# Optimization experiments

Hardware: AMD Instinct MI355X
Metric: run time of the kernel (lower is better)

Reference implementation:

```python
import jax, jax.numpy as jnp
import numpy as np

NEG_SLOPE = 0.2  # PyG GATConv default negative_slope


def gat_layer(x, src, dst, N, W, att_src, att_dst, bias, heads, out_ch, concat):
    # x: [N, Fin]; W: [Fin, heads*out_ch]; att_*: [heads, out_ch]; bias matches output dim
    h = (x @ W).reshape(N, heads, out_ch)              # [N, H, C]
    a_src = (h * att_src).sum(-1)                      # [N, H]
    a_dst = (h * att_dst).sum(-1)                      # [N, H]
    e = jax.nn.leaky_relu(a_src[src] + a_dst[dst], NEG_SLOPE)  # [E, H]
    # segment softmax over incoming edges of each destination node
    e_max = jax.ops.segment_max(e, dst, num_segments=N)        # [N, H]
    e_exp = jnp.exp(e - e_max[dst])                             # [E, H]
    denom = jax.ops.segment_sum(e_exp, dst, num_segments=N)    # [N, H]
    alpha = e_exp / (denom[dst] + 1e-16)                        # [E, H]
    msg = alpha[:, :, None] * h[src]                            # [E, H, C]
    out = jax.ops.segment_sum(msg, dst, num_segments=N)        # [N, H, C]
    out = out.reshape(N, heads * out_ch) if concat else out.mean(axis=1)
    return out + bias


def setup_inputs() -> dict:
    key = jax.random.key(0)
    ks = jax.random.split(key, 10)
    N, E = 40000, 160000
    Fin, H1, C1 = 602, 8, 256
    H2, C2 = 1, 42
    g = lambda k, shape, fan: (jax.random.normal(k, shape, dtype=jnp.float32) * (1.0 / np.sqrt(fan)))
    return {
        "x": jax.random.normal(ks[0], (N, Fin), dtype=jnp.float32),
        "edge_index": jax.random.randint(ks[1], (2, E), 0, N, dtype=jnp.int64),
        "W1": g(ks[2], (Fin, H1 * C1), Fin),
        "att_src1": g(ks[3], (H1, C1), C1),
        "att_dst1": g(ks[4], (H1, C1), C1),
        "b1": jnp.zeros((H1 * C1,), dtype=jnp.float32),
        "W2": g(ks[5], (H1 * C1, H2 * C2), H1 * C1),
        "att_src2": g(ks[6], (H2, C2), C2),
        "att_dst2": g(ks[7], (H2, C2), C2),
        "b2": jnp.zeros((C2,), dtype=jnp.float32),
    }


def reference(x, edge_index, W1, att_src1, att_dst1, b1, W2, att_src2, att_dst2, b2):
    N = x.shape[0]
    # PyG GATConv default add_self_loops=True
    loops = jnp.arange(N, dtype=edge_index.dtype)
    src = jnp.concatenate([edge_index[0], loops])
    dst = jnp.concatenate([edge_index[1], loops])
    h = gat_layer(x, src, dst, N, W1, att_src1, att_dst1, b1, heads=8, out_ch=256, concat=True)
    h = jax.nn.relu(h)  # dropout is identity in eval mode
    h = gat_layer(h, src, dst, N, W2, att_src2, att_dst2, b2, heads=1, out_ch=42, concat=False)
    return jax.nn.log_softmax(h, axis=1)
```

## Files before the change

kernel.cpp:

```cpp
#include <hip/hip_runtime.h>
#include <hip/hip_bf16.h>

#define NN   40000
#define NE   160000
#define ETOT 200000
#define FIN  602
#define NH1  8
#define C1   256
#define F1   2048
#define C2   42
#define NEG  0.2f
#define NB   157
#define KP   608
#define MP   40192

typedef unsigned short u16;
typedef unsigned int   u32;
typedef __bf16 bf16x8 __attribute__((ext_vector_type(8)));
typedef float  f32x4  __attribute__((ext_vector_type(4)));

__device__ __forceinline__ float bfu(u16 v){ return __uint_as_float(((u32)v) << 16); }
__device__ __forceinline__ float bflo(u32 u){ return __uint_as_float(u << 16); }
__device__ __forceinline__ float bfhi(u32 u){ return __uint_as_float(u & 0xffff0000u); }
__device__ __forceinline__ u16 f2bf(float f){
  u32 u = __float_as_uint(f);
  u32 r = (u + 0x7fffu + ((u >> 16) & 1u)) >> 16;
  return (u16)r;
}

__device__ __forceinline__ void gl_lds16(const u16* g, u16* l) {
  __builtin_amdgcn_global_load_lds(
      (const __attribute__((address_space(1))) u32*)(g),
      (__attribute__((address_space(3))) u32*)(l), 16, 0, 0);
}

__global__ void probe_k(const u32* __restrict__ xw, const int* __restrict__ ei,
                        int* __restrict__ flags) {
  if (threadIdx.x == 0) {
    int zc = 0;
    for (int k = 0; k < 64; ++k) zc += (ei[2*k + 1] == 0) ? 1 : 0;
    flags[0] = (zc == 64) ? 1 : 0;
    int inr = 0;
    for (int k = 0; k < 64; ++k) {
      u32 low = xw[k] & 0xffffu;
      int e = (int)((low >> 7) & 0xff);
      inr += (e >= 100 && e <= 140) ? 1 : 0;
    }
    flags[1] = (inr >= 32) ? 0 : 1;
  }
}

__global__ void cvt_f32_k(const void* __restrict__ src, float* __restrict__ dst, int n,
                          const int* __restrict__ flags) {
  int i = blockIdx.x * 256 + threadIdx.x;
  if (i >= n) return;
  dst[i] = flags[1] ? ((const float*)src)[i] : bfu(((const u16*)src)[i]);
}

__global__ void xb_k(const void* __restrict__ x, u16* __restrict__ xb,
                     const int* __restrict__ flags) {
  int k = blockIdx.x * 256 + threadIdx.x;
  int row = blockIdx.y;
  if (k >= KP) return;
  u16 v = 0;
  if (row < NN && k < FIN)
    v = flags[1] ? f2bf(((const float*)x)[(size_t)row * FIN + k])
                 : ((const u16*)x)[(size_t)row * FIN + k];
  xb[(size_t)row * KP + k] = v;
}

__global__ void w1t_k(const void* __restrict__ W1, u16* __restrict__ w1t,
                      const int* __restrict__ flags) {
  int n = blockIdx.x * 256 + threadIdx.x;
  int k = blockIdx.y;
  if (n >= F1) return;
  u16 v = 0;
  if (k < FIN) v = flags[1] ? f2bf(((const float*)W1)[(size_t)k * F1 + n])
                            : ((const u16*)W1)[(size_t)k * F1 + n];
  w1t[(size_t)n * KP + k] = v;
}

__global__ void w2t_k(const void* __restrict__ W2, u16* __restrict__ w2t,
                      const int* __restrict__ flags) {
  int i = blockIdx.x * 256 + threadIdx.x;
  if (i >= 64 * F1) return;
  int c = i >> 11, k = i & (F1 - 1);
  u16 v = 0;
  if (c < C2) v = flags[1] ? f2bf(((const float*)W2)[(size_t)k * C2 + c])
                           : ((const u16*)W2)[(size_t)k * C2 + c];
  w2t[i] = v;
}

__device__ __forceinline__ void edge_sd(const int* __restrict__ ei, int e, int imode,
                                        int& s, int& d) {
  if (e < NE) {
    if (imode) { s = ei[2*e]; d = ei[2*(NE + e)]; }
    else       { s = ei[e];   d = ei[NE + e];     }
  } else { s = d = e - NE; }
}

__global__ void deg_k(const int* __restrict__ ei, int* __restrict__ deg,
                      const int* __restrict__ flags) {
  int e = blockIdx.x * 256 + threadIdx.x;
  if (e >= ETOT) return;
  int s, d; edge_sd(ei, e, flags[0], s, d);
  atomicAdd(&deg[d], 1);
}

__global__ __launch_bounds__(256) void scan1_k(const int* __restrict__ deg,
                                               int* __restrict__ tmp, int* __restrict__ bsum) {
  __shared__ int s[256];
  int b = blockIdx.x, t = threadIdx.x, i = b * 256 + t;
  int v = (i < NN) ? deg[i] : 0;
  s[t] = v; __syncthreads();
  for (int o = 1; o < 256; o <<= 1) {
    int u = (t >= o) ? s[t - o] : 0;
    __syncthreads(); s[t] += u; __syncthreads();
  }
  if (i < NN) tmp[i] = s[t];
  if (t == 255) bsum[b] = s[255];
}

__global__ __launch_bounds__(256) void scan2_k(int* __restrict__ bsum) {
  __shared__ int s[256];
  int t = threadIdx.x;
  int v = (t < NB) ? bsum[t] : 0;
  s[t] = v; __syncthreads();
  for (int o = 1; o < 256; o <<= 1) {
    int u = (t >= o) ? s[t - o] : 0;
    __syncthreads(); s[t] += u; __syncthreads();
  }
  if (t < NB) bsum[t] = s[t];
}

__global__ void scan3_k(const int* __restrict__ deg, const int* __restrict__ tmp,
                        const int* __restrict__ bsum, int* __restrict__ start, int* __restrict__ cur) {
  int i = blockIdx.x * 256 + threadIdx.x;
  if (i >= NN) return;
  int b = i >> 8;
  int off = b ? bsum[b - 1] : 0;
  int excl = tmp[i] - deg[i] + off;
  start[i] = excl; cur[i] = excl;
}

__global__ void fill_k(const int* __restrict__ ei, int* __restrict__ cur,
                       int* __restrict__ csr_src, int* __restrict__ csr_dst,
                       const int* __restrict__ flags) {
  int e = blockIdx.x * 256 + threadIdx.x;
  if (e >= ETOT) return;
  int s, d; edge_sd(ei, e, flags[0], s, d);
  int pos = atomicAdd(&cur[d], 1);
  csr_src[pos] = s; csr_dst[pos] = d;
}

__global__ __launch_bounds__(512) void gemm1c_k(const u16* __restrict__ xb,
                                                const u16* __restrict__ w1t,
                                                u16* __restrict__ h1,
                                                const float* __restrict__ as1c,
                                                const float* __restrict__ ad1c,
                                                float* __restrict__ a_s1,
                                                float* __restrict__ a_d1) {
  __shared__ u16 As[2 * 8192];
  __shared__ u16 Bs[2 * 8192];
  const int t = threadIdx.x;
  const int lane = t & 63, wid = t >> 6;
  const int wr = wid >> 2, wc = wid & 3;
  const int m0 = blockIdx.y * 256, n0 = blockIdx.x * 256;
  const int l16 = lane & 15;
  f32x4 acc[8][4];
  #pragma unroll
  for (int i = 0; i < 8; ++i)
    #pragma unroll
    for (int j = 0; j < 4; ++j) acc[i][j] = (f32x4){0.f, 0.f, 0.f, 0.f};

  const int kc = ((t & 3) ^ ((t >> 3) & 3)) * 8;
  const size_t sa0 = (size_t)(m0 + (t >> 2)) * KP + kc;
  const size_t sa1 = sa0 + (size_t)128 * KP;
  const size_t sb0 = (size_t)(n0 + (t >> 2)) * KP + kc;
  const size_t sb1 = sb0 + (size_t)128 * KP;

  const int fsw = ((lane >> 4) ^ ((l16 >> 1) & 3)) << 3;
  const int rdA = (wr * 128 + l16) * 32 + fsw;
  const int rdB = (wc * 64 + l16) * 32 + fsw;

#define STAGE(K0, B) do {                                  \
    u16* a_ = As + (B) * 8192 + (wid << 9);                \
    u16* b_ = Bs + (B) * 8192 + (wid << 9);                \
    gl_lds16(xb  + sa0 + (K0), a_);                        \
    gl_lds16(xb  + sa1 + (K0), a_ + 4096);                 \
    gl_lds16(w1t + sb0 + (K0), b_);                        \
    gl_lds16(w1t + sb1 + (K0), b_ + 4096);                 \
  } while (0)

  STAGE(0, 0);
  __syncthreads();
  int cur = 0;
  for (int k0 = 0; k0 < KP; k0 += 32) {
    if (k0 + 32 < KP) STAGE(k0 + 32, cur ^ 1);
    const u16* Ab = As + cur * 8192;
    const u16* Bb = Bs + cur * 8192;
    bf16x8 bfr[4];
    #pragma unroll
    for (int ni = 0; ni < 4; ++ni)
      bfr[ni] = *(const bf16x8*)&Bb[rdB + ni * 512];
    #pragma unroll
    for (int mi = 0; mi < 8; ++mi) {
      bf16x8 af = *(const bf16x8*)&Ab[rdA + mi * 512];
      #pragma unroll
      for (int ni = 0; ni < 4; ++ni)
        acc[mi][ni] = __builtin_amdgcn_mfma_f32_16x16x32_bf16(af, bfr[ni], acc[mi][ni], 0, 0, 0);
    }
    __syncthreads();
    cur ^= 1;
  }
#undef STAGE

  const int h0 = n0 >> 8;
  const int lr4 = (lane >> 4) * 4;
  #pragma unroll
  for (int mi = 0; mi < 8; ++mi) {
    float ps[4] = {0.f, 0.f, 0.f, 0.f}, pd[4] = {0.f, 0.f, 0.f, 0.f};
    #pragma unroll
    for (int ni = 0; ni < 4; ++ni) {
      int col = n0 + wc * 64 + ni * 16 + l16;
      float wsv = as1c[col], wdv = ad1c[col];
      #pragma unroll
      for (int r = 0; r < 4; ++r) {
        float v = acc[mi][ni][r];
        ps[r] += v * wsv;
        pd[r] += v * wdv;
      }
    }
    #pragma unroll
    for (int o = 1; o < 16; o <<= 1) {
      #pragma unroll
      for (int r = 0; r < 4; ++r) {
        ps[r] += __shfl_xor(ps[r], o, 64);
        pd[r] += __shfl_xor(pd[r], o, 64);
      }
    }
    int rowb = m0 + wr * 128 + mi * 16 + lr4;
    if (l16 == 0) {
      #pragma unroll
      for (int r = 0; r < 4; ++r) {
        int row = rowb + r;
        if (row < NN) {
          atomicAdd(&a_s1[row * NH1 + h0], ps[r]);
          atomicAdd(&a_d1[row * NH1 + h0], pd[r]);
        }
      }
    }
    #pragma unroll
    for (int r = 0; r < 4; ++r) {
      int row = rowb + r;
      if (row < NN) {
        #pragma unroll
        for (int ni = 0; ni < 4; ++ni) {
          int col = n0 + wc * 64 + ni * 16 + l16;
          h1[(size_t)row * F1 + col] = f2bf(acc[mi][ni][r]);
        }
      }
    }
  }
}

__global__ __launch_bounds__(256) void gemm1m_k(const void* __restrict__ xv,
                                                const u16* __restrict__ w1t,
                                                u16* __restrict__ h1,
                                                const int* __restrict__ flags) {
  __shared__ u16 As[128][40];
  __shared__ u16 Bs[128][40];
  const int fm = flags[1];
  const int t = threadIdx.x;
  const int lane = t & 63, wid = t >> 6;
  const int wr = wid >> 1, wc = wid & 1;
  const int m0 = blockIdx.y * 128, n0 = blockIdx.x * 128;
  const int l16 = lane & 15, lk = (lane >> 4) * 8;
  f32x4 acc[4][4];
  #pragma unroll
  for (int i = 0; i < 4; ++i)
    #pragma unroll
    for (int j = 0; j < 4; ++j) acc[i][j] = (f32x4){0.f, 0.f, 0.f, 0.f};
  const int arow = t >> 2;
  const int akb  = (t & 3) * 8;
  for (int k0 = 0; k0 < KP; k0 += 32) {
    #pragma unroll
    for (int i = 0; i < 2; ++i) {
      int row = arow + i * 64;
      int rg = m0 + row;
      u32 d0 = 0, d1 = 0, d2 = 0, d3 = 0;
      if (rg < NN) {
        if (k0 + 32 <= FIN) {
          if (fm) {
            const float* xp = (const float*)xv + (size_t)rg * FIN + k0 + akb;
            float2 p0 = *(const float2*)(xp);
            float2 p1 = *(const float2*)(xp + 2);
            float2 p2 = *(const float2*)(xp + 4);
            float2 p3 = *(const float2*)(xp + 6);
            d0 = (u32)f2bf(p0.x) | ((u32)f2bf(p0.y) << 16);
            d1 = (u32)f2bf(p1.x) | ((u32)f2bf(p1.y) << 16);
            d2 = (u32)f2bf(p2.x) | ((u32)f2bf(p2.y) << 16);
            d3 = (u32)f2bf(p3.x) | ((u32)f2bf(p3.y) << 16);
          } else {
            const u16* xp = (const u16*)xv + (size_t)rg * FIN + k0 + akb;
            d0 = *(const u32*)(xp);
            d1 = *(const u32*)(xp + 2);
            d2 = *(const u32*)(xp + 4);
            d3 = *(const u32*)(xp + 6);
          }
        } else {
          u16 e[8];
          #pragma unroll
          for (int q = 0; q < 8; ++q) {
            int k = k0 + akb + q;
            e[q] = 0;
            if (k < FIN)
              e[q] = fm ? f2bf(((const float*)xv)[(size_t)rg * FIN + k])
                        : ((const u16*)xv)[(size_t)rg * FIN + k];
          }
          d0 = (u32)e[0] | ((u32)e[1] << 16);
          d1 = (u32)e[2] | ((u32)e[3] << 16);
          d2 = (u32)e[4] | ((u32)e[5] << 16);
          d3 = (u32)e[6] | ((u32)e[7] << 16);
        }
      }
      *(uint4*)&As[row][akb] = make_uint4(d0, d1, d2, d3);
      const u16* wp = w1t + (size_t)(n0 + row) * KP + k0 + akb;
      *(uint4*)&Bs[row][akb] = *(const uint4*)wp;
    }
    __syncthreads();
    bf16x8 bfr[4];
    #pragma unroll
    for (int ni = 0; ni < 4; ++ni)
      bfr[ni] = *(const bf16x8*)&Bs[wc * 64 + ni * 16 + l16][lk];
    #pragma unroll
    for (int mi = 0; mi < 4; ++mi) {
      bf16x8 af = *(const bf16x8*)&As[wr * 64 + mi * 16 + l16][lk];
      #pragma unroll
      for (int ni = 0; ni < 4; ++ni)
        acc[mi][ni] = __builtin_amdgcn_mfma_f32_16x16x32_bf16(af, bfr[ni], acc[mi][ni], 0, 0, 0);
    }
    __syncthreads();
  }
  const int lr4 = (lane >> 4) * 4;
  #pragma unroll
  for (int mi = 0; mi < 4; ++mi) {
    #pragma unroll
    for (int r = 0; r < 4; ++r) {
      int row = m0 + wr * 64 + mi * 16 + lr4 + r;
      if (row < NN) {
        #pragma unroll
        for (int ni = 0; ni < 4; ++ni) {
          int col = n0 + wc * 64 + ni * 16 + l16;
          h1[(size_t)row * F1 + col] = f2bf(acc[mi][ni][r]);
        }
      }
    }
  }
}

__global__ __launch_bounds__(256) void att1_k(const u16* __restrict__ h1,
                                              const float* __restrict__ as1c, const float* __restrict__ ad1c,
                                              float* __restrict__ a_s, float* __restrict__ a_d) {
  int n = blockIdx.x, t = threadIdx.x;
  int h = t >> 5, l = t & 31;
  int base = h * C1 + l * 8;
  const u16* hp = h1 + (size_t)n * F1 + base;
  uint4 v = *(const uint4*)hp;
  u32 w[4] = {v.x, v.y, v.z, v.w};
  float ss = 0.f, sd = 0.f;
  #pragma unroll
  for (int p = 0; p < 4; ++p) {
    float e0 = bflo(w[p]), e1 = bfhi(w[p]);
    ss += e0 * as1c[base + 2*p] + e1 * as1c[base + 2*p + 1];
    sd += e0 * ad1c[base + 2*p] + e1 * ad1c[base + 2*p + 1];
  }
  #pragma unroll
  for (int o = 16; o > 0; o >>= 1) {
    ss += __shfl_down(ss, o, 32);
    sd += __shfl_down(sd, o, 32);
  }
  if (l == 0) { a_s[n * NH1 + h] = ss; a_d[n * NH1 + h] = sd; }
}

__global__ __launch_bounds__(512) void gfuse_k(const int* __restrict__ start, const int* __restrict__ deg,
                                               const int* __restrict__ csr_src,
                                               const float* __restrict__ a_s1, const float* __restrict__ a_d1,
                                               const u16* __restrict__ h1, const float* __restrict__ b1c,
                                               const u16* __restrict__ w2t, float* __restrict__ h2) {
  __shared__ u16 rowsL[16 * F1];
  __shared__ float pb[4][16][16];
  int t = threadIdx.x;
  int nb = blockIdx.x * 16;
  int sub = t & 255, grp = t >> 8;
  int h = sub >> 5;
  int c0 = sub * 8;
  float4 bA = *(const float4*)(b1c + c0);
  float4 bB = *(const float4*)(b1c + c0 + 4);
  for (int ii = 0; ii < 8; ++ii) {
    int i = grp * 8 + ii;
    int n = nb + i;
    int s0 = start[n], jend = s0 + deg[n];
    float ad = a_d1[n * NH1 + h];
    float a0=0.f,a1=0.f,a2=0.f,a3=0.f,a4=0.f,a5=0.f,a6=0.f,a7=0.f,den=0.f;
    int j = s0;
    for (; j + 2 <= jend; j += 2) {
      int sA = csr_src[j], sB = csr_src[j + 1];
      float vA = a_s1[sA * NH1 + h] + ad;
      float vB = a_s1[sB * NH1 + h] + ad;
      vA = vA > 0.f ? vA : NEG * vA;
      vB = vB > 0.f ? vB : NEG * vB;
      float eA = expf(vA), eB = expf(vB);
      uint4 uA = *(const uint4*)(h1 + (size_t)sA * F1 + c0);
      uint4 uB = *(const uint4*)(h1 + (size_t)sB * F1 + c0);
      den += eA + eB;
      a0 += eA * bflo(uA.x) + eB * bflo(uB.x);
      a1 += eA * bfhi(uA.x) + eB * bfhi(uB.x);
      a2 += eA * bflo(uA.y) + eB * bflo(uB.y);
      a3 += eA * bfhi(uA.y) + eB * bfhi(uB.y);
      a4 += eA * bflo(uA.z) + eB * bflo(uB.z);
      a5 += eA * bfhi(uA.z) + eB * bfhi(uB.z);
      a6 += eA * bflo(uA.w) + eB * bflo(uB.w);
      a7 += eA * bfhi(uA.w) + eB * bfhi(uB.w);
    }
    if (j < jend) {
      int sA = csr_src[j];
      float vA = a_s1[sA * NH1 + h] + ad;
      vA = vA > 0.f ? vA : NEG * vA;
      float eA = expf(vA);
      uint4 uA = *(const uint4*)(h1 + (size_t)sA * F1 + c0);
      den += eA;
      a0 += eA * bflo(uA.x); a1 += eA * bfhi(uA.x);
      a2 += eA * bflo(uA.y); a3 += eA * bfhi(uA.y);
      a4 += eA * bflo(uA.z); a5 += eA * bfhi(uA.z);
      a6 += eA * bflo(uA.w); a7 += eA * bfhi(uA.w);
    }
    float inv = 1.f / (den + 1e-16f);
    u16 o0 = f2bf(fmaxf(a0 * inv + bA.x, 0.f));
    u16 o1 = f2bf(fmaxf(a1 * inv + bA.y, 0.f));
    u16 o2 = f2bf(fmaxf(a2 * inv + bA.z, 0.f));
    u16 o3 = f2bf(fmaxf(a3 * inv + bA.w, 0.f));
    u16 o4 = f2bf(fmaxf(a4 * inv + bB.x, 0.f));
    u16 o5 = f2bf(fmaxf(a5 * inv + bB.y, 0.f));
    u16 o6 = f2bf(fmaxf(a6 * inv + bB.z, 0.f));
    u16 o7 = f2bf(fmaxf(a7 * inv + bB.w, 0.f));
    uint4 pk;
    pk.x = (u32)o0 | ((u32)o1 << 16);
    pk.y = (u32)o2 | ((u32)o3 << 16);
    pk.z = (u32)o4 | ((u32)o5 << 16);
    pk.w = (u32)o6 | ((u32)o7 << 16);
    int sw = (i & 7) << 3;
    *(uint4*)&rowsL[i * F1 + (c0 ^ sw)] = pk;
  }
  __syncthreads();
  int lane = t & 63, wid = t >> 6;
  int g = wid & 3, kh = wid >> 2;
  int l16 = lane & 15, lk = (lane >> 4) * 8;
  const u16* wt = w2t + (size_t)(g * 16 + l16) * F1;
  int sw = (l16 & 7) << 3;
  f32x4 acc2 = (f32x4){0.f, 0.f, 0.f, 0.f};
  const int kbase = kh * (F1 / 2);
  for (int k0 = 0; k0 < F1 / 2; k0 += 32) {
    int kk = kbase + k0 + lk;
    bf16x8 af = *(const bf16x8*)&rowsL[l16 * F1 + (kk ^ sw)];
    bf16x8 bf = *(const bf16x8*)(wt + kk);
    acc2 = __builtin_amdgcn_mfma_f32_16x16x32_bf16(af, bf, acc2, 0, 0, 0);
  }
  int mb = (lane >> 4) * 4;
  if (kh == 1) {
    #pragma unroll
    for (int r = 0; r < 4; ++r) pb[g][mb + r][l16] = acc2[r];
  }
  __syncthreads();
  if (kh == 0) {
    int col = g * 16 + l16;
    if (col < C2) {
      #pragma unroll
      for (int r = 0; r < 4; ++r)
        h2[(size_t)(nb + mb + r) * C2 + col] = acc2[r] + pb[g][mb + r][l16];
    }
  }
}

__global__ __launch_bounds__(64) void att2_k(const float* __restrict__ h2,
                                             const float* __restrict__ as2, const float* __restrict__ ad2,
                                             float* __restrict__ a_s, float* __restrict__ a_d) {
  int n = blockIdx.x, t = threadIdx.x;
  float ss = 0.f, sd = 0.f;
  if (t < C2) {
    float v = h2[(size_t)n * C2 + t];
    ss = v * as2[t];
    sd = v * ad2[t];
  }
  #pragma unroll
  for (int o = 32; o > 0; o >>= 1) {
    ss += __shfl_down(ss, o, 64);
    sd += __shfl_down(sd, o, 64);
  }
  if (t == 0) { a_s[n] = ss; a_d[n] = sd; }
}

__global__ __launch_bounds__(64) void gath2_k(const int* __restrict__ start, const int* __restrict__ deg,
                                              const int* __restrict__ csr_src,
                                              const float* __restrict__ a_s, const float* __restrict__ a_d,
                                              const float* __restrict__ h2, const float* __restrict__ b2,
                                              void* __restrict__ outv, const int* __restrict__ flags) {
  int n = blockIdx.x, t = threadIdx.x;
  int s0 = start[n], cnt = deg[n];
  float ad = a_d[n];
  float acc = 0.f, den = 0.f;
  for (int j = s0; j < s0 + cnt; ++j) {
    int s = csr_src[j];
    float v = a_s[s] + ad;
    v = v > 0.f ? v : NEG * v;
    float e = expf(v);
    den += e;
    if (t < C2) acc += e * h2[(size_t)s * C2 + t];
  }
  float raw = (t < C2) ? acc / (den + 1e-16f) + b2[t] : -1e30f;
  float m = raw;
  #pragma unroll
  for (int o = 32; o > 0; o >>= 1) m = fmaxf(m, __shfl_down(m, o, 64));
  m = __shfl(m, 0, 64);
  float e2 = (t < C2) ? expf(raw - m) : 0.f;
  float ssum = e2;
  #pragma unroll
  for (int o = 32; o > 0; o >>= 1) ssum += __shfl_down(ssum, o, 64);
  ssum = __shfl(ssum, 0, 64);
  if (t < C2) {
    float v = raw - m - logf(ssum);
    if (flags[1]) ((float*)outv)[(size_t)n * C2 + t] = v;
    else          ((u16*) outv)[(size_t)n * C2 + t] = f2bf(v);
  }
}

extern "C" void kernel_launch(void* const* d_in, const int* in_sizes, int n_in,
                              void* d_out, int out_size, void* d_ws, size_t ws_size,
                              hipStream_t stream) {
  const void* x   = d_in[0];
  const int*  ei  = (const int*)d_in[1];
  const void* W1  = d_in[2];
  const void* as1 = d_in[3];
  const void* ad1 = d_in[4];
  const void* b1  = d_in[5];
  const void* W2  = d_in[6];
  const void* as2 = d_in[7];
  const void* ad2 = d_in[8];
  const void* b2  = d_in[9];

  char* ws = (char*)d_ws;
  u16*   h1      = (u16*)  (ws);
  float* h2      = (float*)(ws + 163840000);
  float* a_s1    = (float*)(ws + 170560000);
  float* a_d1    = (float*)(ws + 171840000);
  float* a_s2    = (float*)(ws + 173120000);
  float* a_d2    = (float*)(ws + 173280000);
  int*   deg     = (int*)  (ws + 173440000);
  int*   start   = (int*)  (ws + 173600000);
  int*   cur     = (int*)  (ws + 173760000);
  int*   tmp     = (int*)  (ws + 173920000);
  int*   csr_src = (int*)  (ws + 174080000);
  int*   csr_dst = (int*)  (ws + 174880000);
  int*   bsum    = (int*)  (ws + 175680000);
  u16*   w1t     = (u16*)  (ws + 175681024);
  u16*   w2t     = (u16*)  (ws + 178171392);
  float* as1c    = (float*)(ws + 178433536);
  float* ad1c    = (float*)(ws + 178441728);
  float* b1c     = (float*)(ws + 178449920);
  float* as2c    = (float*)(ws + 178458112);
  float* ad2c    = (float*)(ws + 178458368);
  float* b2c     = (float*)(ws + 178458624);
  int*   flags   = (int*)  (ws + 178458880);
  const size_t TOTAL_BASE = 178459136;
  u16*   xb      = (u16*)  (ws + TOTAL_BASE);
  const size_t TOTAL_A = TOTAL_BASE + (size_t)MP * KP * 2;
  if (ws_size < TOTAL_BASE) return;
  const bool pathA = (ws_size >= TOTAL_A);

  probe_k<<<1, 64, 0, stream>>>((const u32*)x, ei, flags);

  cvt_f32_k<<<(F1 + 255) / 256, 256, 0, stream>>>(as1, as1c, F1, flags);
  cvt_f32_k<<<(F1 + 255) / 256, 256, 0, stream>>>(ad1, ad1c, F1, flags);
  cvt_f32_k<<<(F1 + 255) / 256, 256, 0, stream>>>(b1, b1c, F1, flags);
  cvt_f32_k<<<1, 256, 0, stream>>>(as2, as2c, C2, flags);
  cvt_f32_k<<<1, 256, 0, stream>>>(ad2, ad2c, C2, flags);
  cvt_f32_k<<<1, 256, 0, stream>>>(b2, b2c, C2, flags);
  w1t_k<<<dim3(8, KP), 256, 0, stream>>>(W1, w1t, flags);
  w2t_k<<<(64 * F1 + 255) / 256, 256, 0, stream>>>(W2, w2t, flags);

  hipMemsetAsync(deg, 0, NN * sizeof(int), stream);
  hipMemsetAsync(a_s1, 0, 2 * NN * NH1 * sizeof(float), stream);
  const int EB = (ETOT + 255) / 256;
  deg_k  <<<EB, 256, 0, stream>>>(ei, deg, flags);
  scan1_k<<<NB, 256, 0, stream>>>(deg, tmp, bsum);
  scan2_k<<<1, 256, 0, stream>>>(bsum);
  scan3_k<<<NB, 256, 0, stream>>>(deg, tmp, bsum, start, cur);
  fill_k <<<EB, 256, 0, stream>>>(ei, cur, csr_src, csr_dst, flags);

  if (pathA) {
    xb_k<<<dim3((KP + 255) / 256, MP), 256, 0, stream>>>(x, xb, flags);
    gemm1c_k<<<dim3(8, MP / 256), 512, 0, stream>>>(xb, w1t, h1, as1c, ad1c, a_s1, a_d1);
  } else {
    gemm1m_k<<<dim3(16, 313), 256, 0, stream>>>(x, w1t, h1, flags);
    att1_k<<<NN, 256, 0, stream>>>(h1, as1c, ad1c, a_s1, a_d1);
  }
  gfuse_k<<<NN / 16, 512, 0, stream>>>(start, deg, csr_src, a_s1, a_d1, h1, b1c, w2t, h2);

  att2_k<<<NN, 64, 0, stream>>>(h2, as2c, ad2c, a_s2, a_d2);
  gath2_k<<<NN, 64, 0, stream>>>(start, deg, csr_src, a_s2, a_d2, h2, b2c, d_out, flags);
}
```

Measured before the change: 641.7 us.

## Stage GEMM1 output through LDS for coalesced stores; shrink gfuse block to 256 threads

The GEMM1 epilogue now writes bf16 results into shared memory one 16-row slice at a time and copies them out as 32-byte vector stores per row, replacing scattered 2-byte global stores. The fused aggregation kernel drops from 512 to 256 threads. Each thread now handles all 16 nodes and each wave runs the full-K MFMA loop, which removes the split-K partial-sum exchange and its extra barrier. The costs are extra LDS round trips and barriers in the epilogue, and less parallelism per block in gfuse.

```diff
diff --git a/kernel.cpp b/kernel.cpp
--- a/kernel.cpp
+++ b/kernel.cpp
@@ -13,6 +13,7 @@
 #define NB   157
 #define KP   608
 #define MP   40192
+#define CSS  264
 
 typedef unsigned short u16;
 typedef unsigned int   u32;
@@ -239,8 +240,8 @@
         pd[r] += __shfl_xor(pd[r], o, 64);
       }
     }
-    int rowb = m0 + wr * 128 + mi * 16 + lr4;
     if (l16 == 0) {
+      int rowb = m0 + wr * 128 + mi * 16 + lr4;
       #pragma unroll
       for (int r = 0; r < 4; ++r) {
         int row = rowb + r;
@@ -250,16 +251,25 @@
         }
       }
     }
-    #pragma unroll
-    for (int r = 0; r < 4; ++r) {
-      int row = rowb + r;
-      if (row < NN) {
-        #pragma unroll
-        for (int ni = 0; ni < 4; ++ni) {
-          int col = n0 + wc * 64 + ni * 16 + l16;
-          h1[(size_t)row * F1 + col] = f2bf(acc[mi][ni][r]);
-        }
-      }
+  }
+
+  u16* Cs = As;
+  const int rrow = t >> 4;
+  const int rchk = t & 15;
+  for (int mi = 0; mi < 8; ++mi) {
+    __syncthreads();
+    #pragma unroll
+    for (int ni = 0; ni < 4; ++ni)
+      #pragma unroll
+      for (int r = 0; r < 4; ++r)
+        Cs[(wr * 16 + lr4 + r) * CSS + wc * 64 + ni * 16 + l16] = f2bf(acc[mi][ni][r]);
+    __syncthreads();
+    int grow = m0 + (rrow >> 4) * 128 + mi * 16 + (rrow & 15);
+    if (grow < NN) {
+      const uint4* src = (const uint4*)&Cs[rrow * CSS + rchk * 16];
+      uint4 v0 = src[0], v1 = src[1];
+      uint4* dst = (uint4*)&h1[(size_t)grow * F1 + n0 + rchk * 16];
+      dst[0] = v0; dst[1] = v1;
     }
   }
 }
@@ -383,22 +393,19 @@
   if (l == 0) { a_s[n * NH1 + h] = ss; a_d[n * NH1 + h] = sd; }
 }
 
-__global__ __launch_bounds__(512) void gfuse_k(const int* __restrict__ start, const int* __restrict__ deg,
+__global__ __launch_bounds__(256) void gfuse_k(const int* __restrict__ start, const int* __restrict__ deg,
                                                const int* __restrict__ csr_src,
                                                const float* __restrict__ a_s1, const float* __restrict__ a_d1,
                                                const u16* __restrict__ h1, const float* __restrict__ b1c,
                                                const u16* __restrict__ w2t, float* __restrict__ h2) {
   __shared__ u16 rowsL[16 * F1];
-  __shared__ float pb[4][16][16];
   int t = threadIdx.x;
   int nb = blockIdx.x * 16;
-  int sub = t & 255, grp = t >> 8;
-  int h = sub >> 5;
-  int c0 = sub * 8;
+  int h = t >> 5;
+  int c0 = t * 8;
   float4 bA = *(const float4*)(b1c + c0);
   float4 bB = *(const float4*)(b1c + c0 + 4);
-  for (int ii = 0; ii < 8; ++ii) {
-    int i = grp * 8 + ii;
+  for (int i = 0; i < 16; ++i) {
     int n = nb + i;
     int s0 = start[n], jend = s0 + deg[n];
     float ad = a_d1[n * NH1 + h];
@@ -454,31 +461,22 @@
   }
   __syncthreads();
   int lane = t & 63, wid = t >> 6;
-  int g = wid & 3, kh = wid >> 2;
   int l16 = lane & 15, lk = (lane >> 4) * 8;
-  const u16* wt = w2t + (size_t)(g * 16 + l16) * F1;
+  const u16* wt = w2t + (size_t)(wid * 16 + l16) * F1;
   int sw = (l16 & 7) << 3;
   f32x4 acc2 = (f32x4){0.f, 0.f, 0.f, 0.f};
-  const int kbase = kh * (F1 / 2);
-  for (int k0 = 0; k0 < F1 / 2; k0 += 32) {
-    int kk = kbase + k0 + lk;
+  for (int k0 = 0; k0 < F1; k0 += 32) {
+    int kk = k0 + lk;
     bf16x8 af = *(const bf16x8*)&rowsL[l16 * F1 + (kk ^ sw)];
     bf16x8 bf = *(const bf16x8*)(wt + kk);
     acc2 = __builtin_amdgcn_mfma_f32_16x16x32_bf16(af, bf, acc2, 0, 0, 0);
   }
-  int mb = (lane >> 4) * 4;
-  if (kh == 1) {
-    #pragma unroll
-    for (int r = 0; r < 4; ++r) pb[g][mb + r][l16] = acc2[r];
-  }
-  __syncthreads();
-  if (kh == 0) {
-    int col = g * 16 + l16;
-    if (col < C2) {
-      #pragma unroll
-      for (int r = 0; r < 4; ++r)
-        h2[(size_t)(nb + mb + r) * C2 + col] = acc2[r] + pb[g][mb + r][l16];
-    }
+  int col = wid * 16 + l16;
+  if (col < C2) {
+    int mb = (lane >> 4) * 4;
+    #pragma unroll
+    for (int r = 0; r < 4; ++r)
+      h2[(size_t)(nb + mb + r) * C2 + col] = acc2[r];
   }
 }
 
@@ -604,7 +602,7 @@
     gemm1m_k<<<dim3(16, 313), 256, 0, stream>>>(x, w1t, h1, flags);
     att1_k<<<NN, 256, 0, stream>>>(h1, as1c, ad1c, a_s1, a_d1);
   }
-  gfuse_k<<<NN / 16, 512, 0, stream>>>(start, deg, csr_src, a_s1, a_d1, h1, b1c, w2t, h2);
+  gfuse_k<<<NN / 16, 256, 0, stream>>>(start, deg, csr_src, a_s1, a_d1, h1, b1c, w2t, h2);
 
   att2_k<<<NN, 64, 0, stream>>>(h2, as2c, ad2c, a_s2, a_d2);
   gath2_k<<<NN, 64, 0, stream>>>(start, deg, csr_src, a_s2, a_d2, h2, b2c, d_out, flags);
```

New measurement: 647.7 us. No clear change (+0.9%).
